# Kernel optimization log

Hardware: AMD Instinct MI355X
Metric: run time of the kernel (lower is better)

Reference implementation:

```python
import jax, jax.numpy as jnp
import numpy as np

B, S, D, H = 2, 2048, 1024, 16
HD = D // H


def setup_inputs() -> dict:
    key = jax.random.key(0)
    ks = jax.random.split(key, 9)
    x = jax.random.normal(ks[0], (B, S, D), dtype=jnp.float32)
    scale = 1.0 / np.sqrt(D)
    Wq = jax.random.normal(ks[1], (D, D), dtype=jnp.float32) * scale
    bq = jnp.zeros((D,), dtype=jnp.float32)
    Wk = jax.random.normal(ks[2], (D, D), dtype=jnp.float32) * scale
    bk = jnp.zeros((D,), dtype=jnp.float32)
    Wv = jax.random.normal(ks[3], (D, D), dtype=jnp.float32) * scale
    bv = jnp.zeros((D,), dtype=jnp.float32)
    Wo = jax.random.normal(ks[4], (D, D), dtype=jnp.float32) * scale
    bo = jnp.zeros((D,), dtype=jnp.float32)
    return {"x": x, "Wq": Wq, "bq": bq, "Wk": Wk, "bk": bk,
            "Wv": Wv, "bv": bv, "Wo": Wo, "bo": bo}


def reference(x, Wq, bq, Wk, bk, Wv, bv, Wo, bo):
    b, s, d = x.shape
    h, hd = H, HD
    # torch Linear: y = x @ W.T + b
    q = (x @ Wq.T + bq).reshape(b, s, h, hd).transpose(0, 2, 1, 3)  # (b,h,s,hd)
    k = (x @ Wk.T + bk).reshape(b, s, h, hd).transpose(0, 2, 1, 3)
    v = (x @ Wv.T + bv).reshape(b, s, h, hd).transpose(0, 2, 1, 3)
    scores = jnp.einsum('bhqd,bhkd->bhqk', q, k) / np.sqrt(hd)  # (b,h,s,s)
    # FAITHFUL to source: softmax over dim=1 (head axis), not the key axis.
    attn = jax.nn.softmax(scores, axis=1)
    # dropout is identity at inference
    out = jnp.einsum('bhqk,bhkd->bhqd', attn, v)  # (b,h,s,hd)
    out = out.transpose(0, 2, 1, 3).reshape(b, s, d)
    return out @ Wo.T + bo
```

## Files before the change

kernel.cpp:

```cpp
#include <hip/hip_runtime.h>
#include <hip/hip_bf16.h>
#include <cstdint>
#include <cstddef>


typedef __bf16 bf16x8 __attribute__((ext_vector_type(8)));
typedef __bf16 bf16x4 __attribute__((ext_vector_type(4)));
typedef _Float16 f16x4 __attribute__((ext_vector_type(4)));
typedef _Float16 f16x8 __attribute__((ext_vector_type(8)));
typedef float floatx4 __attribute__((ext_vector_type(4)));

#define S_LEN 2048
#define DIM 1024
#define NH 16
#define HD 64
#define MTOT 4096

__device__ __forceinline__ void g2l16(const void* g, void* l) {
    __builtin_amdgcn_global_load_lds(
        (const __attribute__((address_space(1))) void*)g,
        (__attribute__((address_space(3))) void*)l, 16, 0, 0);
}

__global__ void cast_f32_bf16(const float* __restrict__ s, __bf16* __restrict__ d, int n) {
    int i = (blockIdx.x * blockDim.x + threadIdx.x) * 4;
    if (i < n) {
        float4 v = *(const float4*)&s[i];
        bf16x4 o;
        o.x = (__bf16)v.x; o.y = (__bf16)v.y; o.z = (__bf16)v.z; o.w = (__bf16)v.w;
        *(bf16x4*)&d[i] = o;
    }
}

template <typename OUT_T>
__global__ __launch_bounds__(256, 2) void gemm_bt2(const __bf16* __restrict__ A,
                                                   const __bf16* __restrict__ Bw,
                                                   const float* __restrict__ bias,
                                                   OUT_T* __restrict__ C,
                                                   int M, int N, int K) {
    const int tm = blockIdx.y * 128, tn = blockIdx.x * 64;
    __shared__ __bf16 As[2 * 128 * 32];
    __shared__ __bf16 Bs[2 * 64 * 32];
    const int tid = threadIdx.x, wid = tid >> 6, lane = tid & 63;
    const int l15 = lane & 15, quad = lane >> 4;
    const int wm = (wid >> 1) * 64, wn = (wid & 1) * 32;
    floatx4 acc[4][2] = {};
    for (int k0 = 0; k0 < K; k0 += 64) {
        __syncthreads();
#pragma unroll
        for (int i = 0; i < 4; ++i) {
            int slot = i * 256 + tid;
            int p = slot >> 9, r = (slot >> 2) & 127, c8 = (slot & 3) * 8;
            g2l16(&A[(size_t)(tm + r) * K + k0 + p * 32 + c8], &As[slot * 8]);
        }
#pragma unroll
        for (int i = 0; i < 2; ++i) {
            int slot = i * 256 + tid;
            int p = slot >> 8, r = (slot >> 2) & 63, c8 = (slot & 3) * 8;
            g2l16(&Bw[(size_t)(tn + r) * K + k0 + p * 32 + c8], &Bs[slot * 8]);
        }
        __syncthreads();
#pragma unroll
        for (int kc = 0; kc < 2; ++kc) {
            bf16x8 af[4], bf[2];
#pragma unroll
            for (int t = 0; t < 4; ++t)
                af[t] = *(const bf16x8*)&As[kc * 4096 + (wm + t * 16 + l15) * 32 + quad * 8];
#pragma unroll
            for (int t = 0; t < 2; ++t)
                bf[t] = *(const bf16x8*)&Bs[kc * 2048 + (wn + t * 16 + l15) * 32 + quad * 8];
#pragma unroll
            for (int im = 0; im < 4; ++im)
#pragma unroll
                for (int in = 0; in < 2; ++in)
                    acc[im][in] = __builtin_amdgcn_mfma_f32_16x16x32_bf16(af[im], bf[in], acc[im][in], 0, 0, 0);
        }
    }
#pragma unroll
    for (int im = 0; im < 4; ++im)
#pragma unroll
        for (int in = 0; in < 2; ++in)
#pragma unroll
            for (int r = 0; r < 4; ++r) {
                int row = tm + wm + im * 16 + quad * 4 + r;
                int col = tn + wn + in * 16 + l15;
                C[(size_t)row * N + col] = (OUT_T)(acc[im][in][r] + bias[col]);
            }
}

__global__ void transpose16(const ushort* __restrict__ src, ushort* __restrict__ dst,
                            int M, int N) {
    __shared__ ushort t[32][33];
    int bx = blockIdx.x * 32, by = blockIdx.y * 32;
    int x = threadIdx.x, y = threadIdx.y;
#pragma unroll
    for (int i = 0; i < 32; i += 8) t[y + i][x] = src[(size_t)(by + y + i) * N + bx + x];
    __syncthreads();
#pragma unroll
    for (int i = 0; i < 32; i += 8) dst[(size_t)(bx + y + i) * M + by + x] = t[x][y + i];
}

__global__ __launch_bounds__(256, 4) void den2(const __bf16* __restrict__ Q,
                                               const __bf16* __restrict__ Km,
                                               __bf16* __restrict__ rd) {
    const int kt = blockIdx.x * 128, qt = blockIdx.y * 64, b = blockIdx.z;
    __shared__ __bf16 Qs[2 * 64 * 32];
    __shared__ __bf16 Ks[2 * 128 * 32];
    const int tid = threadIdx.x, wid = tid >> 6, lane = tid & 63;
    const int l15 = lane & 15, quad = lane >> 4;
    const int wq = wid * 16;
    floatx4 dsum[8] = {};
    for (int h = 0; h < NH; ++h) {
        __syncthreads();
#pragma unroll
        for (int i = 0; i < 2; ++i) {
            int slot = i * 256 + tid;
            int p = slot >> 8, r = (slot >> 2) & 63, c8 = (slot & 3) * 8;
            g2l16(&Q[(size_t)(b * S_LEN + qt + r) * DIM + h * HD + p * 32 + c8], &Qs[slot * 8]);
        }
#pragma unroll
        for (int i = 0; i < 4; ++i) {
            int slot = i * 256 + tid;
            int p = slot >> 9, r = (slot >> 2) & 127, c8 = (slot & 3) * 8;
            g2l16(&Km[(size_t)(b * S_LEN + kt + r) * DIM + h * HD + p * 32 + c8], &Ks[slot * 8]);
        }
        __syncthreads();
        bf16x8 af0 = *(const bf16x8*)&Qs[(wq + l15) * 32 + quad * 8];
        bf16x8 af1 = *(const bf16x8*)&Qs[2048 + (wq + l15) * 32 + quad * 8];
#pragma unroll
        for (int n = 0; n < 8; ++n) {
            bf16x8 b0 = *(const bf16x8*)&Ks[(n * 16 + l15) * 32 + quad * 8];
            bf16x8 b1 = *(const bf16x8*)&Ks[4096 + (n * 16 + l15) * 32 + quad * 8];
            floatx4 acc = {};
            acc = __builtin_amdgcn_mfma_f32_16x16x32_bf16(af0, b0, acc, 0, 0, 0);
            acc = __builtin_amdgcn_mfma_f32_16x16x32_bf16(af1, b1, acc, 0, 0, 0);
#pragma unroll
            for (int r = 0; r < 4; ++r) dsum[n][r] += __expf(acc[r] * 0.125f);
        }
    }
#pragma unroll
    for (int n = 0; n < 8; ++n)
#pragma unroll
        for (int r = 0; r < 4; ++r) {
            int q = qt + wq + quad * 4 + r;
            int k = kt + n * 16 + l15;
            rd[(size_t)(b * S_LEN + q) * S_LEN + k] = (__bf16)(1.0f / dsum[n][r]);
        }
}

__global__ __launch_bounds__(256, 2) void attn2(const __bf16* __restrict__ Q,
                                                const __bf16* __restrict__ Km,
                                                const _Float16* __restrict__ Vt,
                                                const __bf16* __restrict__ rd,
                                                __bf16* __restrict__ AO) {
    const int qt = blockIdx.x * 128, h = blockIdx.y, b = blockIdx.z;
    __shared__ __bf16 Ks[2 * 128 * 32];
    __shared__ __bf16 rds[128 * 136];
    __shared__ _Float16 Vts[64 * 136];
    const int tid = threadIdx.x, wid = tid >> 6, lane = tid & 63;
    const int l15 = lane & 15, quad = lane >> 4;
    const int wq = wid * 32;
    bf16x8 qf[2][2];
#pragma unroll
    for (int np = 0; np < 2; ++np)
#pragma unroll
        for (int kc = 0; kc < 2; ++kc)
            qf[np][kc] = *(const bf16x8*)&Q[(size_t)(b * S_LEN + qt + wq + np * 16 + l15) * DIM +
                                            h * HD + kc * 32 + quad * 8];
    floatx4 oacc[2][4] = {};
    for (int kt = 0; kt < S_LEN; kt += 128) {
        __syncthreads();
#pragma unroll
        for (int i = 0; i < 4; ++i) {
            int slot = i * 256 + tid;
            int p = slot >> 9, r = (slot >> 2) & 127, c8 = (slot & 3) * 8;
            g2l16(&Km[(size_t)(b * S_LEN + kt + r) * DIM + h * HD + p * 32 + c8], &Ks[slot * 8]);
        }
#pragma unroll
        for (int i = 0; i < 8; ++i) {
            int slot = i * 256 + tid;
            int r = slot >> 4, c = (slot & 15) * 8;
            *(bf16x8*)&rds[r * 136 + c] =
                *(const bf16x8*)&rd[(size_t)(b * S_LEN + qt + r) * S_LEN + kt + c];
        }
#pragma unroll
        for (int i = 0; i < 4; ++i) {
            int slot = i * 256 + tid;
            int r = slot >> 4, c = (slot & 15) * 8;
            *(f16x8*)&Vts[r * 136 + c] =
                *(const f16x8*)&Vt[(size_t)(h * HD + r) * MTOT + b * S_LEN + kt + c];
        }
        __syncthreads();
#pragma unroll
        for (int mp = 0; mp < 8; ++mp) {
            bf16x8 kf0 = *(const bf16x8*)&Ks[(mp * 16 + l15) * 32 + quad * 8];
            bf16x8 kf1 = *(const bf16x8*)&Ks[4096 + (mp * 16 + l15) * 32 + quad * 8];
            floatx4 s0 = {}, s1 = {};
            s0 = __builtin_amdgcn_mfma_f32_16x16x32_bf16(kf0, qf[0][0], s0, 0, 0, 0);
            s0 = __builtin_amdgcn_mfma_f32_16x16x32_bf16(kf1, qf[0][1], s0, 0, 0, 0);
            s1 = __builtin_amdgcn_mfma_f32_16x16x32_bf16(kf0, qf[1][0], s1, 0, 0, 0);
            s1 = __builtin_amdgcn_mfma_f32_16x16x32_bf16(kf1, qf[1][1], s1, 0, 0, 0);
            bf16x4 rv0 = *(const bf16x4*)&rds[(wq + l15) * 136 + mp * 16 + quad * 4];
            bf16x4 rv1 = *(const bf16x4*)&rds[(wq + 16 + l15) * 136 + mp * 16 + quad * 4];
            f16x4 pa0, pa1;
#pragma unroll
            for (int r = 0; r < 4; ++r) {
                pa0[r] = (_Float16)(__expf(s0[r] * 0.125f) * (float)rv0[r]);
                pa1[r] = (_Float16)(__expf(s1[r] * 0.125f) * (float)rv1[r]);
            }
#pragma unroll
            for (int n = 0; n < 4; ++n) {
                f16x4 vb = *(const f16x4*)&Vts[(n * 16 + l15) * 136 + mp * 16 + quad * 4];
                oacc[0][n] = __builtin_amdgcn_mfma_f32_16x16x16f16(pa0, vb, oacc[0][n], 0, 0, 0);
                oacc[1][n] = __builtin_amdgcn_mfma_f32_16x16x16f16(pa1, vb, oacc[1][n], 0, 0, 0);
            }
        }
    }
#pragma unroll
    for (int np = 0; np < 2; ++np)
#pragma unroll
        for (int n = 0; n < 4; ++n)
#pragma unroll
            for (int r = 0; r < 4; ++r) {
                int row = qt + wq + np * 16 + quad * 4 + r;
                int col = h * HD + n * 16 + l15;
                AO[(size_t)(b * S_LEN + row) * DIM + col] = (__bf16)oacc[np][n][r];
            }
}

extern "C" void kernel_launch(void* const* d_in, const int* in_sizes, int n_in,
                              void* d_out, int out_size, void* d_ws, size_t ws_size,
                              hipStream_t stream) {
    const float* x  = (const float*)d_in[0];
    const float* Wq = (const float*)d_in[1];
    const float* bq = (const float*)d_in[2];
    const float* Wk = (const float*)d_in[3];
    const float* bk = (const float*)d_in[4];
    const float* Wv = (const float*)d_in[5];
    const float* bv = (const float*)d_in[6];
    const float* Wo = (const float*)d_in[7];
    const float* bo = (const float*)d_in[8];
    float* out = (float*)d_out;

    char* ws = (char*)d_ws;
    const size_t MB = 1u << 20;
    __bf16*    xb  = (__bf16*)(ws);
    __bf16*    Wqb = (__bf16*)(ws + 8 * MB);
    __bf16*    Wkb = (__bf16*)(ws + 10 * MB);
    __bf16*    Wvb = (__bf16*)(ws + 12 * MB);
    __bf16*    Wob = (__bf16*)(ws + 14 * MB);
    __bf16*    Qb  = (__bf16*)(ws + 16 * MB);
    __bf16*    Kb  = (__bf16*)(ws + 24 * MB);
    _Float16*  Vh  = (_Float16*)(ws + 32 * MB);
    _Float16*  VtH = (_Float16*)(ws + 40 * MB);
    __bf16*    rd  = (__bf16*)(ws + 48 * MB);
    __bf16*    AOb = (__bf16*)(ws + 64 * MB);

    cast_f32_bf16<<<4096, 256, 0, stream>>>(x,  xb,  MTOT * DIM);
    cast_f32_bf16<<<1024, 256, 0, stream>>>(Wq, Wqb, DIM * DIM);
    cast_f32_bf16<<<1024, 256, 0, stream>>>(Wk, Wkb, DIM * DIM);
    cast_f32_bf16<<<1024, 256, 0, stream>>>(Wv, Wvb, DIM * DIM);
    cast_f32_bf16<<<1024, 256, 0, stream>>>(Wo, Wob, DIM * DIM);

    dim3 gproj(DIM / 64, MTOT / 128);
    gemm_bt2<__bf16><<<gproj, 256, 0, stream>>>(xb, Wqb, bq, Qb, MTOT, DIM, DIM);
    gemm_bt2<__bf16><<<gproj, 256, 0, stream>>>(xb, Wkb, bk, Kb, MTOT, DIM, DIM);
    gemm_bt2<_Float16><<<gproj, 256, 0, stream>>>(xb, Wvb, bv, Vh, MTOT, DIM, DIM);

    dim3 gtr(DIM / 32, MTOT / 32);
    transpose16<<<gtr, dim3(32, 8), 0, stream>>>((const ushort*)Vh, (ushort*)VtH, MTOT, DIM);

    dim3 gden(S_LEN / 128, S_LEN / 64, 2);
    den2<<<gden, 256, 0, stream>>>(Qb, Kb, rd);

    dim3 gattn(S_LEN / 128, NH, 2);
    attn2<<<gattn, 256, 0, stream>>>(Qb, Kb, VtH, rd, AOb);

    gemm_bt2<float><<<gproj, 256, 0, stream>>>(AOb, Wob, bo, out, MTOT, DIM, DIM);
}
```

Baseline: 310.7 us.

## Fuse QKV projections with transposed V store, merge weight casts, retile attention kernels

Merges the four weight-cast launches into one, and fuses the Q/K/V projection GEMMs into a single launch that writes V directly in transposed fp16 layout, removing the separate transpose kernel. The denominator kernel now loads K for two heads per iteration and reads Q fragments straight from global memory instead of staging them in LDS. The attention kernel drops the LDS staging of the reciprocal-denominator tile, reads it directly from global, and halves its query tile so it can run higher occupancy. Together these cut launch count and intermediate traffic, at the cost of uncoalesced direct global reads of rd and Q and a strided Vt store pattern.

```diff
diff --git a/kernel.cpp b/kernel.cpp
--- a/kernel.cpp
+++ b/kernel.cpp
@@ -32,12 +32,109 @@
     }
 }
 
-template <typename OUT_T>
-__global__ __launch_bounds__(256, 2) void gemm_bt2(const __bf16* __restrict__ A,
+__global__ void cast_w4(const float* __restrict__ w0, const float* __restrict__ w1,
+                        const float* __restrict__ w2, const float* __restrict__ w3,
+                        __bf16* __restrict__ o0, __bf16* __restrict__ o1,
+                        __bf16* __restrict__ o2, __bf16* __restrict__ o3, int n) {
+    const float* s; __bf16* d;
+    switch (blockIdx.y) {
+        case 0: s = w0; d = o0; break;
+        case 1: s = w1; d = o1; break;
+        case 2: s = w2; d = o2; break;
+        default: s = w3; d = o3; break;
+    }
+    int i = (blockIdx.x * blockDim.x + threadIdx.x) * 4;
+    if (i < n) {
+        float4 v = *(const float4*)&s[i];
+        bf16x4 o;
+        o.x = (__bf16)v.x; o.y = (__bf16)v.y; o.z = (__bf16)v.z; o.w = (__bf16)v.w;
+        *(bf16x4*)&d[i] = o;
+    }
+}
+
+__global__ __launch_bounds__(256, 4) void qkv_gemm(const __bf16* __restrict__ A,
+                                                   const __bf16* __restrict__ Wq,
+                                                   const __bf16* __restrict__ Wk,
+                                                   const __bf16* __restrict__ Wv,
+                                                   const float* __restrict__ bq,
+                                                   const float* __restrict__ bk,
+                                                   const float* __restrict__ bv,
+                                                   __bf16* __restrict__ Qo,
+                                                   __bf16* __restrict__ Ko,
+                                                   _Float16* __restrict__ Vt) {
+    const int tng = blockIdx.x * 64, tm = blockIdx.y * 128;
+    const int wsel = tng >> 10, tn = tng & 1023;
+    const __bf16* W = (wsel == 0) ? Wq : (wsel == 1) ? Wk : Wv;
+    const float* bias = (wsel == 0) ? bq : (wsel == 1) ? bk : bv;
+    __shared__ __bf16 As[2 * 128 * 32];
+    __shared__ __bf16 Bs[2 * 64 * 32];
+    const int tid = threadIdx.x, wid = tid >> 6, lane = tid & 63;
+    const int l15 = lane & 15, quad = lane >> 4;
+    const int wm = (wid >> 1) * 64, wn = (wid & 1) * 32;
+    floatx4 acc[4][2] = {};
+    for (int k0 = 0; k0 < DIM; k0 += 64) {
+        __syncthreads();
+#pragma unroll
+        for (int i = 0; i < 4; ++i) {
+            int slot = i * 256 + tid;
+            int p = slot >> 9, r = (slot >> 2) & 127, c8 = (slot & 3) * 8;
+            g2l16(&A[(size_t)(tm + r) * DIM + k0 + p * 32 + c8], &As[slot * 8]);
+        }
+#pragma unroll
+        for (int i = 0; i < 2; ++i) {
+            int slot = i * 256 + tid;
+            int p = slot >> 8, r = (slot >> 2) & 63, c8 = (slot & 3) * 8;
+            g2l16(&W[(size_t)(tn + r) * DIM + k0 + p * 32 + c8], &Bs[slot * 8]);
+        }
+        __syncthreads();
+#pragma unroll
+        for (int kc = 0; kc < 2; ++kc) {
+            bf16x8 af[4], bf[2];
+#pragma unroll
+            for (int t = 0; t < 4; ++t)
+                af[t] = *(const bf16x8*)&As[kc * 4096 + (wm + t * 16 + l15) * 32 + quad * 8];
+#pragma unroll
+            for (int t = 0; t < 2; ++t)
+                bf[t] = *(const bf16x8*)&Bs[kc * 2048 + (wn + t * 16 + l15) * 32 + quad * 8];
+#pragma unroll
+            for (int im = 0; im < 4; ++im)
+#pragma unroll
+                for (int in = 0; in < 2; ++in)
+                    acc[im][in] = __builtin_amdgcn_mfma_f32_16x16x32_bf16(af[im], bf[in], acc[im][in], 0, 0, 0);
+        }
+    }
+    if (wsel < 2) {
+        __bf16* O = wsel ? Ko : Qo;
+#pragma unroll
+        for (int im = 0; im < 4; ++im)
+#pragma unroll
+            for (int in = 0; in < 2; ++in)
+#pragma unroll
+                for (int r = 0; r < 4; ++r) {
+                    int row = tm + wm + im * 16 + quad * 4 + r;
+                    int col = tn + wn + in * 16 + l15;
+                    O[(size_t)row * DIM + col] = (__bf16)(acc[im][in][r] + bias[col]);
+                }
+    } else {
+#pragma unroll
+        for (int im = 0; im < 4; ++im)
+#pragma unroll
+            for (int in = 0; in < 2; ++in) {
+                int cv = tn + wn + in * 16 + l15;
+                int row4 = tm + wm + im * 16 + quad * 4;
+                float bv_ = bias[cv];
+                f16x4 o;
+#pragma unroll
+                for (int r = 0; r < 4; ++r) o[r] = (_Float16)(acc[im][in][r] + bv_);
+                *(f16x4*)&Vt[(size_t)cv * MTOT + row4] = o;
+            }
+    }
+}
+
+__global__ __launch_bounds__(256, 2) void gemm_out(const __bf16* __restrict__ A,
                                                    const __bf16* __restrict__ Bw,
                                                    const float* __restrict__ bias,
-                                                   OUT_T* __restrict__ C,
-                                                   int M, int N, int K) {
+                                                   float* __restrict__ C) {
     const int tm = blockIdx.y * 128, tn = blockIdx.x * 64;
     __shared__ __bf16 As[2 * 128 * 32];
     __shared__ __bf16 Bs[2 * 64 * 32];
@@ -45,19 +142,19 @@
     const int l15 = lane & 15, quad = lane >> 4;
     const int wm = (wid >> 1) * 64, wn = (wid & 1) * 32;
     floatx4 acc[4][2] = {};
-    for (int k0 = 0; k0 < K; k0 += 64) {
+    for (int k0 = 0; k0 < DIM; k0 += 64) {
         __syncthreads();
 #pragma unroll
         for (int i = 0; i < 4; ++i) {
             int slot = i * 256 + tid;
             int p = slot >> 9, r = (slot >> 2) & 127, c8 = (slot & 3) * 8;
-            g2l16(&A[(size_t)(tm + r) * K + k0 + p * 32 + c8], &As[slot * 8]);
+            g2l16(&A[(size_t)(tm + r) * DIM + k0 + p * 32 + c8], &As[slot * 8]);
         }
 #pragma unroll
         for (int i = 0; i < 2; ++i) {
             int slot = i * 256 + tid;
             int p = slot >> 8, r = (slot >> 2) & 63, c8 = (slot & 3) * 8;
-            g2l16(&Bw[(size_t)(tn + r) * K + k0 + p * 32 + c8], &Bs[slot * 8]);
+            g2l16(&Bw[(size_t)(tn + r) * DIM + k0 + p * 32 + c8], &Bs[slot * 8]);
         }
         __syncthreads();
 #pragma unroll
@@ -84,58 +181,46 @@
             for (int r = 0; r < 4; ++r) {
                 int row = tm + wm + im * 16 + quad * 4 + r;
                 int col = tn + wn + in * 16 + l15;
-                C[(size_t)row * N + col] = (OUT_T)(acc[im][in][r] + bias[col]);
+                C[(size_t)row * DIM + col] = acc[im][in][r] + bias[col];
             }
 }
 
-__global__ void transpose16(const ushort* __restrict__ src, ushort* __restrict__ dst,
-                            int M, int N) {
-    __shared__ ushort t[32][33];
-    int bx = blockIdx.x * 32, by = blockIdx.y * 32;
-    int x = threadIdx.x, y = threadIdx.y;
-#pragma unroll
-    for (int i = 0; i < 32; i += 8) t[y + i][x] = src[(size_t)(by + y + i) * N + bx + x];
-    __syncthreads();
-#pragma unroll
-    for (int i = 0; i < 32; i += 8) dst[(size_t)(bx + y + i) * M + by + x] = t[x][y + i];
-}
-
-__global__ __launch_bounds__(256, 4) void den2(const __bf16* __restrict__ Q,
+__global__ __launch_bounds__(256, 4) void den3(const __bf16* __restrict__ Q,
                                                const __bf16* __restrict__ Km,
                                                __bf16* __restrict__ rd) {
     const int kt = blockIdx.x * 128, qt = blockIdx.y * 64, b = blockIdx.z;
-    __shared__ __bf16 Qs[2 * 64 * 32];
-    __shared__ __bf16 Ks[2 * 128 * 32];
+    __shared__ __bf16 Ks[2 * 2 * 128 * 32];
     const int tid = threadIdx.x, wid = tid >> 6, lane = tid & 63;
     const int l15 = lane & 15, quad = lane >> 4;
     const int wq = wid * 16;
     floatx4 dsum[8] = {};
-    for (int h = 0; h < NH; ++h) {
-        __syncthreads();
-#pragma unroll
-        for (int i = 0; i < 2; ++i) {
-            int slot = i * 256 + tid;
-            int p = slot >> 8, r = (slot >> 2) & 63, c8 = (slot & 3) * 8;
-            g2l16(&Q[(size_t)(b * S_LEN + qt + r) * DIM + h * HD + p * 32 + c8], &Qs[slot * 8]);
-        }
-#pragma unroll
-        for (int i = 0; i < 4; ++i) {
-            int slot = i * 256 + tid;
-            int p = slot >> 9, r = (slot >> 2) & 127, c8 = (slot & 3) * 8;
-            g2l16(&Km[(size_t)(b * S_LEN + kt + r) * DIM + h * HD + p * 32 + c8], &Ks[slot * 8]);
-        }
-        __syncthreads();
-        bf16x8 af0 = *(const bf16x8*)&Qs[(wq + l15) * 32 + quad * 8];
-        bf16x8 af1 = *(const bf16x8*)&Qs[2048 + (wq + l15) * 32 + quad * 8];
-#pragma unroll
-        for (int n = 0; n < 8; ++n) {
-            bf16x8 b0 = *(const bf16x8*)&Ks[(n * 16 + l15) * 32 + quad * 8];
-            bf16x8 b1 = *(const bf16x8*)&Ks[4096 + (n * 16 + l15) * 32 + quad * 8];
-            floatx4 acc = {};
-            acc = __builtin_amdgcn_mfma_f32_16x16x32_bf16(af0, b0, acc, 0, 0, 0);
-            acc = __builtin_amdgcn_mfma_f32_16x16x32_bf16(af1, b1, acc, 0, 0, 0);
-#pragma unroll
-            for (int r = 0; r < 4; ++r) dsum[n][r] += __expf(acc[r] * 0.125f);
+    const size_t qrow = (size_t)(b * S_LEN + qt + wq + l15) * DIM;
+    for (int hh = 0; hh < 8; ++hh) {
+        __syncthreads();
+#pragma unroll
+        for (int i = 0; i < 8; ++i) {
+            int slot = i * 256 + tid;
+            int hs = slot >> 10, rem = slot & 1023;
+            int p = rem >> 9, r = (rem >> 2) & 127, c8 = (rem & 3) * 8;
+            g2l16(&Km[(size_t)(b * S_LEN + kt + r) * DIM + (hh * 2 + hs) * HD + p * 32 + c8],
+                  &Ks[slot * 8]);
+        }
+        __syncthreads();
+#pragma unroll
+        for (int hs = 0; hs < 2; ++hs) {
+            int h = hh * 2 + hs;
+            bf16x8 af0 = *(const bf16x8*)&Q[qrow + h * HD + quad * 8];
+            bf16x8 af1 = *(const bf16x8*)&Q[qrow + h * HD + 32 + quad * 8];
+#pragma unroll
+            for (int n = 0; n < 8; ++n) {
+                bf16x8 b0 = *(const bf16x8*)&Ks[hs * 8192 + (n * 16 + l15) * 32 + quad * 8];
+                bf16x8 b1 = *(const bf16x8*)&Ks[hs * 8192 + 4096 + (n * 16 + l15) * 32 + quad * 8];
+                floatx4 acc = {};
+                acc = __builtin_amdgcn_mfma_f32_16x16x32_bf16(af0, b0, acc, 0, 0, 0);
+                acc = __builtin_amdgcn_mfma_f32_16x16x32_bf16(af1, b1, acc, 0, 0, 0);
+#pragma unroll
+                for (int r = 0; r < 4; ++r) dsum[n][r] += __expf(acc[r] * 0.125f);
+            }
         }
     }
 #pragma unroll
@@ -148,26 +233,22 @@
         }
 }
 
-__global__ __launch_bounds__(256, 2) void attn2(const __bf16* __restrict__ Q,
+__global__ __launch_bounds__(256, 4) void attn3(const __bf16* __restrict__ Q,
                                                 const __bf16* __restrict__ Km,
                                                 const _Float16* __restrict__ Vt,
                                                 const __bf16* __restrict__ rd,
                                                 __bf16* __restrict__ AO) {
-    const int qt = blockIdx.x * 128, h = blockIdx.y, b = blockIdx.z;
+    const int qt = blockIdx.x * 64, h = blockIdx.y, b = blockIdx.z;
     __shared__ __bf16 Ks[2 * 128 * 32];
-    __shared__ __bf16 rds[128 * 136];
     __shared__ _Float16 Vts[64 * 136];
     const int tid = threadIdx.x, wid = tid >> 6, lane = tid & 63;
     const int l15 = lane & 15, quad = lane >> 4;
-    const int wq = wid * 32;
-    bf16x8 qf[2][2];
-#pragma unroll
-    for (int np = 0; np < 2; ++np)
-#pragma unroll
-        for (int kc = 0; kc < 2; ++kc)
-            qf[np][kc] = *(const bf16x8*)&Q[(size_t)(b * S_LEN + qt + wq + np * 16 + l15) * DIM +
-                                            h * HD + kc * 32 + quad * 8];
-    floatx4 oacc[2][4] = {};
+    const int wq = wid * 16;
+    const size_t qrow = (size_t)(b * S_LEN + qt + wq + l15) * DIM + h * HD;
+    bf16x8 qf0 = *(const bf16x8*)&Q[qrow + quad * 8];
+    bf16x8 qf1 = *(const bf16x8*)&Q[qrow + 32 + quad * 8];
+    const __bf16* rdrow = &rd[(size_t)(b * S_LEN + qt + wq + l15) * S_LEN];
+    floatx4 oacc[4] = {};
     for (int kt = 0; kt < S_LEN; kt += 128) {
         __syncthreads();
 #pragma unroll
@@ -175,13 +256,6 @@
             int slot = i * 256 + tid;
             int p = slot >> 9, r = (slot >> 2) & 127, c8 = (slot & 3) * 8;
             g2l16(&Km[(size_t)(b * S_LEN + kt + r) * DIM + h * HD + p * 32 + c8], &Ks[slot * 8]);
-        }
-#pragma unroll
-        for (int i = 0; i < 8; ++i) {
-            int slot = i * 256 + tid;
-            int r = slot >> 4, c = (slot & 15) * 8;
-            *(bf16x8*)&rds[r * 136 + c] =
-                *(const bf16x8*)&rd[(size_t)(b * S_LEN + qt + r) * S_LEN + kt + c];
         }
 #pragma unroll
         for (int i = 0; i < 4; ++i) {
@@ -195,37 +269,29 @@
         for (int mp = 0; mp < 8; ++mp) {
             bf16x8 kf0 = *(const bf16x8*)&Ks[(mp * 16 + l15) * 32 + quad * 8];
             bf16x8 kf1 = *(const bf16x8*)&Ks[4096 + (mp * 16 + l15) * 32 + quad * 8];
-            floatx4 s0 = {}, s1 = {};
-            s0 = __builtin_amdgcn_mfma_f32_16x16x32_bf16(kf0, qf[0][0], s0, 0, 0, 0);
-            s0 = __builtin_amdgcn_mfma_f32_16x16x32_bf16(kf1, qf[0][1], s0, 0, 0, 0);
-            s1 = __builtin_amdgcn_mfma_f32_16x16x32_bf16(kf0, qf[1][0], s1, 0, 0, 0);
-            s1 = __builtin_amdgcn_mfma_f32_16x16x32_bf16(kf1, qf[1][1], s1, 0, 0, 0);
-            bf16x4 rv0 = *(const bf16x4*)&rds[(wq + l15) * 136 + mp * 16 + quad * 4];
-            bf16x4 rv1 = *(const bf16x4*)&rds[(wq + 16 + l15) * 136 + mp * 16 + quad * 4];
-            f16x4 pa0, pa1;
-#pragma unroll
-            for (int r = 0; r < 4; ++r) {
-                pa0[r] = (_Float16)(__expf(s0[r] * 0.125f) * (float)rv0[r]);
-                pa1[r] = (_Float16)(__expf(s1[r] * 0.125f) * (float)rv1[r]);
-            }
+            floatx4 s = {};
+            s = __builtin_amdgcn_mfma_f32_16x16x32_bf16(kf0, qf0, s, 0, 0, 0);
+            s = __builtin_amdgcn_mfma_f32_16x16x32_bf16(kf1, qf1, s, 0, 0, 0);
+            bf16x4 rv = *(const bf16x4*)&rdrow[kt + mp * 16 + quad * 4];
+            f16x4 pa;
+#pragma unroll
+            for (int r = 0; r < 4; ++r)
+                pa[r] = (_Float16)(__expf(s[r] * 0.125f) * (float)rv[r]);
 #pragma unroll
             for (int n = 0; n < 4; ++n) {
                 f16x4 vb = *(const f16x4*)&Vts[(n * 16 + l15) * 136 + mp * 16 + quad * 4];
-                oacc[0][n] = __builtin_amdgcn_mfma_f32_16x16x16f16(pa0, vb, oacc[0][n], 0, 0, 0);
-                oacc[1][n] = __builtin_amdgcn_mfma_f32_16x16x16f16(pa1, vb, oacc[1][n], 0, 0, 0);
+                oacc[n] = __builtin_amdgcn_mfma_f32_16x16x16f16(pa, vb, oacc[n], 0, 0, 0);
             }
         }
     }
 #pragma unroll
-    for (int np = 0; np < 2; ++np)
-#pragma unroll
-        for (int n = 0; n < 4; ++n)
-#pragma unroll
-            for (int r = 0; r < 4; ++r) {
-                int row = qt + wq + np * 16 + quad * 4 + r;
-                int col = h * HD + n * 16 + l15;
-                AO[(size_t)(b * S_LEN + row) * DIM + col] = (__bf16)oacc[np][n][r];
-            }
+    for (int n = 0; n < 4; ++n)
+#pragma unroll
+        for (int r = 0; r < 4; ++r) {
+            int row = qt + wq + quad * 4 + r;
+            int col = h * HD + n * 16 + l15;
+            AO[(size_t)(b * S_LEN + row) * DIM + col] = (__bf16)oacc[n][r];
+        }
 }
 
 extern "C" void kernel_launch(void* const* d_in, const int* in_sizes, int n_in,
@@ -251,30 +317,18 @@
     __bf16*    Wob = (__bf16*)(ws + 14 * MB);
     __bf16*    Qb  = (__bf16*)(ws + 16 * MB);
     __bf16*    Kb  = (__bf16*)(ws + 24 * MB);
-    _Float16*  Vh  = (_Float16*)(ws + 32 * MB);
-    _Float16*  VtH = (_Float16*)(ws + 40 * MB);
-    __bf16*    rd  = (__bf16*)(ws + 48 * MB);
-    __bf16*    AOb = (__bf16*)(ws + 64 * MB);
-
-    cast_f32_bf16<<<4096, 256, 0, stream>>>(x,  xb,  MTOT * DIM);
-    cast_f32_bf16<<<1024, 256, 0, stream>>>(Wq, Wqb, DIM * DIM);
-    cast_f32_bf16<<<1024, 256, 0, stream>>>(Wk, Wkb, DIM * DIM);
-    cast_f32_bf16<<<1024, 256, 0, stream>>>(Wv, Wvb, DIM * DIM);
-    cast_f32_bf16<<<1024, 256, 0, stream>>>(Wo, Wob, DIM * DIM);
-
-    dim3 gproj(DIM / 64, MTOT / 128);
-    gemm_bt2<__bf16><<<gproj, 256, 0, stream>>>(xb, Wqb, bq, Qb, MTOT, DIM, DIM);
-    gemm_bt2<__bf16><<<gproj, 256, 0, stream>>>(xb, Wkb, bk, Kb, MTOT, DIM, DIM);
-    gemm_bt2<_Float16><<<gproj, 256, 0, stream>>>(xb, Wvb, bv, Vh, MTOT, DIM, DIM);
-
-    dim3 gtr(DIM / 32, MTOT / 32);
-    transpose16<<<gtr, dim3(32, 8), 0, stream>>>((const ushort*)Vh, (ushort*)VtH, MTOT, DIM);
-
-    dim3 gden(S_LEN / 128, S_LEN / 64, 2);
-    den2<<<gden, 256, 0, stream>>>(Qb, Kb, rd);
-
-    dim3 gattn(S_LEN / 128, NH, 2);
-    attn2<<<gattn, 256, 0, stream>>>(Qb, Kb, VtH, rd, AOb);
-
-    gemm_bt2<float><<<gproj, 256, 0, stream>>>(AOb, Wob, bo, out, MTOT, DIM, DIM);
-}
+    _Float16*  VtH = (_Float16*)(ws + 32 * MB);
+    __bf16*    rd  = (__bf16*)(ws + 40 * MB);
+    __bf16*    AOb = (__bf16*)(ws + 56 * MB);
+
+    cast_f32_bf16<<<4096, 256, 0, stream>>>(x, xb, MTOT * DIM);
+    cast_w4<<<dim3(1024, 4), 256, 0, stream>>>(Wq, Wk, Wv, Wo, Wqb, Wkb, Wvb, Wob, DIM * DIM);
+
+    qkv_gemm<<<dim3(48, 32), 256, 0, stream>>>(xb, Wqb, Wkb, Wvb, bq, bk, bv, Qb, Kb, VtH);
+
+    den3<<<dim3(S_LEN / 128, S_LEN / 64, 2), 256, 0, stream>>>(Qb, Kb, rd);
+
+    attn3<<<dim3(S_LEN / 64, NH, 2), 256, 0, stream>>>(Qb, Kb, VtH, rd, AOb);
+
+    gemm_out<<<dim3(DIM / 64, MTOT / 128), 256, 0, stream>>>(AOb, Wob, bo, out);
+}
```

After: 282.4 us. 9.1% less time.
